# Kernel optimization log

Hardware: AMD Instinct MI355X
Metric: run time of the kernel (lower is better)

The kernel has to match this reference:

```python
import jax, jax.numpy as jnp
import numpy as np

N = 50000
E = 800000
IN_C = 256
HID = 256
OUT_C = 64
HEADS = 4
NEG_SLOPE = 0.2  # PyG GATConv default leaky_relu slope


def gat_conv(x, edge_index, W, a_src, a_dst, bias, heads, concat):
    """PyG-style GATConv (add_self_loops=True, eval mode so no dropout).
    x: [N, F_in]; W: [F_in, heads*C]; a_src/a_dst: [heads, C]; bias: [heads*C] or [C].
    """
    n = x.shape[0]
    # add self loops
    loops = jnp.arange(n, dtype=edge_index.dtype)
    src = jnp.concatenate([edge_index[0], loops])
    dst = jnp.concatenate([edge_index[1], loops])
    h = (x @ W).reshape(n, heads, -1)               # [N, H, C]
    alpha_src = jnp.einsum('nhc,hc->nh', h, a_src)  # [N, H]
    alpha_dst = jnp.einsum('nhc,hc->nh', h, a_dst)
    e = jax.nn.leaky_relu(alpha_src[src] + alpha_dst[dst], NEG_SLOPE)  # [E', H]
    # segment softmax over incoming edges of each dst node
    m = jax.ops.segment_max(e, dst, num_segments=n)        # [N, H]
    w = jnp.exp(e - m[dst])
    denom = jax.ops.segment_sum(w, dst, num_segments=n)    # [N, H]
    att = w / (denom[dst] + 1e-16)                          # [E', H]
    out = jax.ops.segment_sum(h[src] * att[:, :, None], dst, num_segments=n)  # [N, H, C]
    out = out.reshape(n, -1) if concat else out.mean(axis=1)
    return out + bias


def setup_inputs() -> dict:
    key = jax.random.key(0)
    ks = jax.random.split(key, 10)
    c1 = HID // HEADS  # per-head channels of layer 1
    s_in = 1.0 / np.sqrt(IN_C)
    s_hid = 1.0 / np.sqrt(HID)
    return {
        'x': jax.random.normal(ks[0], (N, IN_C), dtype=jnp.float32),
        'edge_index': jax.random.randint(ks[1], (2, E), 0, N, dtype=jnp.int64),
        'W1': jax.random.normal(ks[2], (IN_C, HEADS * c1), dtype=jnp.float32) * s_in,
        'a_src1': jax.random.normal(ks[3], (HEADS, c1), dtype=jnp.float32) * s_in,
        'a_dst1': jax.random.normal(ks[4], (HEADS, c1), dtype=jnp.float32) * s_in,
        'b1': jnp.zeros((HEADS * c1,), dtype=jnp.float32),
        'W2': jax.random.normal(ks[5], (HID, OUT_C), dtype=jnp.float32) * s_hid,
        'a_src2': jax.random.normal(ks[6], (1, OUT_C), dtype=jnp.float32) * s_hid,
        'a_dst2': jax.random.normal(ks[7], (1, OUT_C), dtype=jnp.float32) * s_hid,
        'b2': jnp.zeros((OUT_C,), dtype=jnp.float32),
    }


def reference(x, edge_index, W1, a_src1, a_dst1, b1, W2, a_src2, a_dst2, b2):
    h = gat_conv(x, edge_index, W1, a_src1, a_dst1, b1, heads=HEADS, concat=True)
    h = jax.nn.elu(h)
    # dropout: eval mode -> identity
    return gat_conv(h, edge_index, W2, a_src2, a_dst2, b2, heads=1, concat=False)
```

## Files before the change

kernel.cpp:

```cpp
#include <hip/hip_runtime.h>
#include <math.h>

#define NN 50000
#define NE 800000
#define ET (NE + NN)
#define FIN 256
#define HIDC 256
#define OC 64
#define NH 4
#define NEG 0.2f
#define CAP 64
#define NSTRIPES (NN / 16)
#define NGROUPS ((NSTRIPES + 1) / 2)

typedef __attribute__((ext_vector_type(8))) short bf16x8;
typedef __attribute__((ext_vector_type(4))) float f32x4;

__device__ __forceinline__ unsigned short f2bf(float f) {
    unsigned u = __float_as_uint(f);
    unsigned r = (u + 0x7FFFu + ((u >> 16) & 1u)) >> 16;
    return (unsigned short)r;
}
__device__ __forceinline__ float bflo(unsigned v) { return __uint_as_float(v << 16); }
__device__ __forceinline__ float bfhi(unsigned v) { return __uint_as_float(v & 0xffff0000u); }

__global__ void k_scatter(const int* __restrict__ ei, int* __restrict__ cnt,
                          unsigned short* __restrict__ esrc) {
    int e = blockIdx.x * blockDim.x + threadIdx.x;
    if (e >= ET) return;
    int s, d;
    if (e < NE) { s = ei[e]; d = ei[NE + e]; } else { s = d = e - NE; }
    int k = atomicAdd(&cnt[d], 1);
    if (k < CAP) esrc[(size_t)d * CAP + k] = (unsigned short)s;
}

__global__ void k_cvt(const float* __restrict__ x, unsigned short* __restrict__ xb,
                      int n) {
    int i = (blockIdx.x * 256 + threadIdx.x) * 8;
    if (i >= n) return;
    float4 f0 = *(const float4*)&x[i];
    float4 f1 = *(const float4*)&x[i + 4];
    uint4 o;
    o.x = (unsigned)f2bf(f0.x) | ((unsigned)f2bf(f0.y) << 16);
    o.y = (unsigned)f2bf(f0.z) | ((unsigned)f2bf(f0.w) << 16);
    o.z = (unsigned)f2bf(f1.x) | ((unsigned)f2bf(f1.y) << 16);
    o.w = (unsigned)f2bf(f1.z) | ((unsigned)f2bf(f1.w) << 16);
    *(uint4*)&xb[i] = o;
}

__global__ void k_pack(const float* __restrict__ W, unsigned short* __restrict__ Bp,
                       int N, int NTL, int total) {
    int t = blockIdx.x * 256 + threadIdx.x;
    if (t >= total) return;
    int lane = t & 63;
    int ntl = (t >> 6) % NTL;
    int ks = ((t >> 6) / NTL) & 7;
    int hy = t / (64 * NTL * 8);
    int col = hy * NTL * 16 + ntl * 16 + (lane & 15);
    int k0 = ks * 32 + (lane >> 4) * 8;
#pragma unroll
    for (int i = 0; i < 8; i++) Bp[(size_t)t * 8 + i] = f2bf(W[(k0 + i) * N + col]);
}

template <int NTL, int NHEADS>
__global__ void __launch_bounds__(256) k_gemm(const unsigned short* __restrict__ A,
                                              const unsigned short* __restrict__ Bp,
                                              unsigned short* __restrict__ D, int N,
                                              const float* __restrict__ aS,
                                              const float* __restrict__ aD,
                                              float* __restrict__ asOut,
                                              float* __restrict__ adOut) {
    constexpr int TOT = 8 * NTL * 64 * 8;
    constexpr int HPH = (NTL * 16) / 64;
    __shared__ unsigned short lds[TOT];
    const unsigned short* src = Bp + (size_t)blockIdx.y * TOT;
    for (int i = threadIdx.x * 8; i < TOT; i += 256 * 8)
        *(uint4*)&lds[i] = *(const uint4*)&src[i];
    __syncthreads();
    int wave = threadIdx.x >> 6, lane = threadIdx.x & 63;
    int l15 = lane & 15, lh = lane >> 4;
    int coloff = blockIdx.y * NTL * 16;
    float aSv[NTL], aDv[NTL];
#pragma unroll
    for (int nt = 0; nt < NTL; nt++) {
        aSv[nt] = aS[coloff + nt * 16 + l15];
        aDv[nt] = aD[coloff + nt * 16 + l15];
    }
    for (int g = blockIdx.x * 4 + wave; g < NGROUPS; g += gridDim.x * 4) {
        int st0 = g * 2;
        bool two = (st0 + 1 < NSTRIPES);
        const unsigned short* arow0 = A + (size_t)(st0 * 16 + l15) * 256 + lh * 8;
        const unsigned short* arow1 = two ? arow0 + 16 * 256 : arow0;
        bf16x8 a0[8], a1[8];
#pragma unroll
        for (int ks = 0; ks < 8; ks++) a0[ks] = *(const bf16x8*)(arow0 + ks * 32);
#pragma unroll
        for (int ks = 0; ks < 8; ks++) a1[ks] = *(const bf16x8*)(arow1 + ks * 32);
        f32x4 acc[2][NTL];
#pragma unroll
        for (int m = 0; m < 2; m++)
#pragma unroll
            for (int t = 0; t < NTL; t++) acc[m][t] = (f32x4){0.f, 0.f, 0.f, 0.f};
#pragma unroll
        for (int ks = 0; ks < 8; ks++) {
#pragma unroll
            for (int nt = 0; nt < NTL; nt++) {
                bf16x8 b = *(const bf16x8*)&lds[((size_t)(ks * NTL + nt) * 64 + lane) * 8];
                acc[0][nt] = __builtin_amdgcn_mfma_f32_16x16x32_bf16(a0[ks], b, acc[0][nt], 0, 0, 0);
                acc[1][nt] = __builtin_amdgcn_mfma_f32_16x16x32_bf16(a1[ks], b, acc[1][nt], 0, 0, 0);
            }
        }
        int nm = two ? 2 : 1;
        for (int m = 0; m < nm; m++) {
            int strow = (st0 + m) * 16;
            unsigned short* dbase = D + (size_t)strow * N + coloff;
#pragma unroll
            for (int nt = 0; nt < NTL; nt++)
#pragma unroll
                for (int r = 0; r < 4; r++)
                    dbase[(lh * 4 + r) * N + nt * 16 + l15] = f2bf(acc[m][nt][r]);
#pragma unroll
            for (int r = 0; r < 4; r++) {
#pragma unroll
                for (int gg = 0; gg < HPH; gg++) {
                    float ps = 0.f, pd = 0.f;
#pragma unroll
                    for (int q = 0; q < 4; q++) {
                        int nt = gg * 4 + q;
                        ps += acc[m][nt][r] * aSv[nt];
                        pd += acc[m][nt][r] * aDv[nt];
                    }
#pragma unroll
                    for (int off = 1; off < 16; off <<= 1) {
                        ps += __shfl_xor(ps, off);
                        pd += __shfl_xor(pd, off);
                    }
                    if (l15 == 0) {
                        int row = strow + lh * 4 + r;
                        int hidx = blockIdx.y * HPH + gg;
                        asOut[row * NHEADS + hidx] = ps;
                        adOut[row * NHEADS + hidx] = pd;
                    }
                }
            }
        }
    }
}


__global__ void k_agg1f(const int* __restrict__ cnt, const unsigned short* __restrict__ esrc,
                        const unsigned short* __restrict__ h, const float* __restrict__ as,
                        const float* __restrict__ ad, const float* __restrict__ bias,
                        unsigned short* __restrict__ out) {
    __shared__ float wlds[4][64][4];
    int wave = threadIdx.x >> 6;
    int n = blockIdx.x * 4 + wave;
    int lane = threadIdx.x & 63;
    if (n >= NN) return;
    int deg = cnt[n];
    deg = deg < CAP ? deg : CAP;
    const unsigned short* bucket = &esrc[(size_t)n * CAP];
    bool act = lane < deg;
    int myS = act ? (int)bucket[lane] : 0;
    float4 adv = *(const float4*)&ad[n * NH];
    float e0 = -INFINITY, e1 = -INFINITY, e2 = -INFINITY, e3 = -INFINITY;
    if (act) {
        float4 av = *(const float4*)&as[myS * NH];
        e0 = av.x + adv.x; e0 = e0 > 0.f ? e0 : NEG * e0;
        e1 = av.y + adv.y; e1 = e1 > 0.f ? e1 : NEG * e1;
        e2 = av.z + adv.z; e2 = e2 > 0.f ? e2 : NEG * e2;
        e3 = av.w + adv.w; e3 = e3 > 0.f ? e3 : NEG * e3;
    }
    float m0 = e0, m1 = e1, m2 = e2, m3 = e3;
    for (int off = 32; off; off >>= 1) {
        m0 = fmaxf(m0, __shfl_xor(m0, off));
        m1 = fmaxf(m1, __shfl_xor(m1, off));
        m2 = fmaxf(m2, __shfl_xor(m2, off));
        m3 = fmaxf(m3, __shfl_xor(m3, off));
    }
    float w0 = act ? expf(e0 - m0) : 0.f;
    float w1 = act ? expf(e1 - m1) : 0.f;
    float w2 = act ? expf(e2 - m2) : 0.f;
    float w3 = act ? expf(e3 - m3) : 0.f;
    *(float4*)&wlds[wave][lane][0] = (float4){w0, w1, w2, w3};
    float s0 = w0, s1 = w1, s2 = w2, s3 = w3;
    for (int off = 32; off; off >>= 1) {
        s0 += __shfl_xor(s0, off);
        s1 += __shfl_xor(s1, off);
        s2 += __shfl_xor(s2, off);
        s3 += __shfl_xor(s3, off);
    }
    int hh = lane >> 4;
    int cbase = hh * 64 + (lane & 15) * 4;
    float ssel = hh == 0 ? s0 : hh == 1 ? s1 : hh == 2 ? s2 : s3;
    float rsel = 1.f / (ssel + 1e-16f);
    const float* wcol = &wlds[wave][0][hh];
    const unsigned short* hb = h + cbase;
    float acc0 = 0.f, acc1 = 0.f, acc2 = 0.f, acc3 = 0.f;
    int degP = (deg + 7) & ~7;
    for (int j = 0; j < degP; j += 8) {
        uint2 pv[8];
        float wj[8];
#pragma unroll
        for (int u = 0; u < 8; u++) {
            int s = __shfl(myS, j + u);
            wj[u] = wcol[(j + u) * 4];
            pv[u] = *(const uint2*)&hb[(size_t)s * HIDC];
        }
#pragma unroll
        for (int u = 0; u < 8; u++) {
            acc0 += wj[u] * bflo(pv[u].x);
            acc1 += wj[u] * bfhi(pv[u].x);
            acc2 += wj[u] * bflo(pv[u].y);
            acc3 += wj[u] * bfhi(pv[u].y);
        }
    }
    float4 bv = *(const float4*)&bias[cbase];
    float v0 = acc0 * rsel + bv.x; v0 = v0 > 0.f ? v0 : expm1f(v0);
    float v1 = acc1 * rsel + bv.y; v1 = v1 > 0.f ? v1 : expm1f(v1);
    float v2 = acc2 * rsel + bv.z; v2 = v2 > 0.f ? v2 : expm1f(v2);
    float v3 = acc3 * rsel + bv.w; v3 = v3 > 0.f ? v3 : expm1f(v3);
    uint2 ov;
    ov.x = (unsigned)f2bf(v0) | ((unsigned)f2bf(v1) << 16);
    ov.y = (unsigned)f2bf(v2) | ((unsigned)f2bf(v3) << 16);
    *(uint2*)&out[(size_t)n * HIDC + cbase] = ov;
}

__global__ void k_agg2f(const int* __restrict__ cnt, const unsigned short* __restrict__ esrc,
                        const unsigned short* __restrict__ h, const float* __restrict__ as,
                        const float* __restrict__ ad, const float* __restrict__ bias,
                        float* __restrict__ out) {
    __shared__ float wlds[4][64];
    int wave = threadIdx.x >> 6;
    int n = blockIdx.x * 4 + wave;
    int lane = threadIdx.x & 63;
    if (n >= NN) return;
    int deg = cnt[n];
    deg = deg < CAP ? deg : CAP;
    const unsigned short* bucket = &esrc[(size_t)n * CAP];
    bool act = lane < deg;
    int myS = act ? (int)bucket[lane] : 0;
    float adv = ad[n];
    float e = -INFINITY;
    if (act) {
        e = as[myS] + adv;
        e = e > 0.f ? e : NEG * e;
    }
    float m = e;
    for (int off = 32; off; off >>= 1) m = fmaxf(m, __shfl_xor(m, off));
    float w = act ? expf(e - m) : 0.f;
    wlds[wave][lane] = w;
    float s = w;
    for (int off = 32; off; off >>= 1) s += __shfl_xor(s, off);
    float rd = 1.f / (s + 1e-16f);

    int sub = lane >> 4;
    int cw = (lane & 15) * 4;
    const unsigned short* hb = h + cw;
    float acc0 = 0.f, acc1 = 0.f, acc2 = 0.f, acc3 = 0.f;
    int degP = (deg + 7) & ~7;
    for (int j = 0; j < degP; j += 8) {
        uint2 pv[2];
        float wj[2];
#pragma unroll
        for (int u = 0; u < 2; u++) {
            int jj = j + u * 4 + sub;
            int sj = __shfl(myS, jj);
            wj[u] = wlds[wave][jj];
            pv[u] = *(const uint2*)&hb[(size_t)sj * OC];
        }
#pragma unroll
        for (int u = 0; u < 2; u++) {
            acc0 += wj[u] * bflo(pv[u].x);
            acc1 += wj[u] * bfhi(pv[u].x);
            acc2 += wj[u] * bflo(pv[u].y);
            acc3 += wj[u] * bfhi(pv[u].y);
        }
    }
#pragma unroll
    for (int off = 16; off < 64; off <<= 1) {
        acc0 += __shfl_xor(acc0, off);
        acc1 += __shfl_xor(acc1, off);
        acc2 += __shfl_xor(acc2, off);
        acc3 += __shfl_xor(acc3, off);
    }
    if (lane < 16) {
        float4 bv = *(const float4*)&bias[cw];
        float4 o;
        o.x = acc0 * rd + bv.x;
        o.y = acc1 * rd + bv.y;
        o.z = acc2 * rd + bv.z;
        o.w = acc3 * rd + bv.w;
        *(float4*)&out[(size_t)n * OC + cw] = o;
    }
}

extern "C" void kernel_launch(void* const* d_in, const int* in_sizes, int n_in,
                              void* d_out, int out_size, void* d_ws, size_t ws_size,
                              hipStream_t stream) {
    const float* x   = (const float*)d_in[0];
    const int*   ei  = (const int*)d_in[1];
    const float* W1  = (const float*)d_in[2];
    const float* aS1 = (const float*)d_in[3];
    const float* aD1 = (const float*)d_in[4];
    const float* b1  = (const float*)d_in[5];
    const float* W2  = (const float*)d_in[6];
    const float* aS2 = (const float*)d_in[7];
    const float* aD2 = (const float*)d_in[8];
    const float* b2  = (const float*)d_in[9];
    float* out = (float*)d_out;

    char* p = (char*)d_ws;
    auto alloc = [&](size_t nbytes) {
        char* r = p;
        p += (nbytes + 255) & ~(size_t)255;
        return r;
    };
    unsigned short* xb    = (unsigned short*)alloc((size_t)NN * FIN * 2);
    unsigned short* h1b   = (unsigned short*)alloc((size_t)NN * HIDC * 2);
    unsigned short* act1b = (unsigned short*)alloc((size_t)NN * HIDC * 2);
    unsigned short* h2b   = (unsigned short*)alloc((size_t)NN * OC * 2);
    unsigned short* Bp1   = (unsigned short*)alloc((size_t)2 * 8 * 8 * 64 * 8 * 2);
    unsigned short* Bp2   = (unsigned short*)alloc((size_t)1 * 8 * 4 * 64 * 8 * 2);
    float* as1  = (float*)alloc((size_t)NN * NH * 4);
    float* ad1  = (float*)alloc((size_t)NN * NH * 4);
    float* as2  = (float*)alloc((size_t)NN * 4);
    float* ad2  = (float*)alloc((size_t)NN * 4);
    int*   cnt  = (int*)alloc((size_t)NN * 4);
    unsigned short* esrc = (unsigned short*)alloc((size_t)NN * CAP * 2);

    hipMemsetAsync(cnt, 0, (size_t)NN * 4, stream);

    k_scatter<<<(ET + 255) / 256, 256, 0, stream>>>(ei, cnt, esrc);
    k_cvt<<<(NN * FIN / 8 + 255) / 256, 256, 0, stream>>>(x, xb, NN * FIN);
    k_pack<<<(2 * 8 * 8 * 64 + 255) / 256, 256, 0, stream>>>(W1, Bp1, HIDC, 8, 2 * 8 * 8 * 64);
    k_pack<<<(1 * 8 * 4 * 64 + 255) / 256, 256, 0, stream>>>(W2, Bp2, OC, 4, 1 * 8 * 4 * 64);

    k_gemm<8, NH><<<dim3(196, 2), 256, 0, stream>>>(xb, Bp1, h1b, HIDC, aS1, aD1, as1, ad1);
    k_agg1f<<<(NN + 3) / 4, 256, 0, stream>>>(cnt, esrc, h1b, as1, ad1, b1, act1b);

    k_gemm<4, 1><<<dim3(196, 1), 256, 0, stream>>>(act1b, Bp2, h2b, OC, aS2, aD2, as2, ad2);
    k_agg2f<<<(NN + 3) / 4, 256, 0, stream>>>(cnt, esrc, h2b, as2, ad2, b2, out);
}
```

Baseline: 226.8 us.

## Split layer-1 aggregation into attention-weight kernel and channel-sliced gather kernel

The fused layer-1 aggregation kernel is split in two. The first kernel computes the softmax attention weights and reciprocal denominators per node and writes them to a new global buffer laid out per head. The second kernel gathers neighbor features with each block covering a 32-channel slice of 8 nodes. This raises parallelism and shrinks the per-thread gather width, which may improve locality of the source-row gathers across slices. The cost is an extra launch, a roughly 51 MB weight buffer written and read back, and narrower 4-byte loads per lane.

```diff
diff --git a/kernel.cpp b/kernel.cpp
--- a/kernel.cpp
+++ b/kernel.cpp
@@ -147,25 +147,21 @@
     }
 }
 
-
-__global__ void k_agg1f(const int* __restrict__ cnt, const unsigned short* __restrict__ esrc,
-                        const unsigned short* __restrict__ h, const float* __restrict__ as,
-                        const float* __restrict__ ad, const float* __restrict__ bias,
-                        unsigned short* __restrict__ out) {
-    __shared__ float wlds[4][64][4];
+__global__ void k_attn1(const int* __restrict__ cnt, const unsigned short* __restrict__ esrc,
+                        const float* __restrict__ as, const float* __restrict__ ad,
+                        float* __restrict__ watt, float* __restrict__ rden) {
     int wave = threadIdx.x >> 6;
     int n = blockIdx.x * 4 + wave;
-    int lane = threadIdx.x & 63;
+    int j = threadIdx.x & 63;
     if (n >= NN) return;
     int deg = cnt[n];
     deg = deg < CAP ? deg : CAP;
-    const unsigned short* bucket = &esrc[(size_t)n * CAP];
-    bool act = lane < deg;
-    int myS = act ? (int)bucket[lane] : 0;
+    bool act = j < deg;
+    int s = act ? (int)esrc[(size_t)n * CAP + j] : 0;
     float4 adv = *(const float4*)&ad[n * NH];
     float e0 = -INFINITY, e1 = -INFINITY, e2 = -INFINITY, e3 = -INFINITY;
     if (act) {
-        float4 av = *(const float4*)&as[myS * NH];
+        float4 av = *(const float4*)&as[s * NH];
         e0 = av.x + adv.x; e0 = e0 > 0.f ? e0 : NEG * e0;
         e1 = av.y + adv.y; e1 = e1 > 0.f ? e1 : NEG * e1;
         e2 = av.z + adv.z; e2 = e2 > 0.f ? e2 : NEG * e2;
@@ -182,7 +178,11 @@
     float w1 = act ? expf(e1 - m1) : 0.f;
     float w2 = act ? expf(e2 - m2) : 0.f;
     float w3 = act ? expf(e3 - m3) : 0.f;
-    *(float4*)&wlds[wave][lane][0] = (float4){w0, w1, w2, w3};
+    size_t base = (size_t)n * CAP + j;
+    watt[base] = w0;
+    watt[(size_t)NN * CAP + base] = w1;
+    watt[(size_t)2 * NN * CAP + base] = w2;
+    watt[(size_t)3 * NN * CAP + base] = w3;
     float s0 = w0, s1 = w1, s2 = w2, s3 = w3;
     for (int off = 32; off; off >>= 1) {
         s0 += __shfl_xor(s0, off);
@@ -190,40 +190,56 @@
         s2 += __shfl_xor(s2, off);
         s3 += __shfl_xor(s3, off);
     }
-    int hh = lane >> 4;
-    int cbase = hh * 64 + (lane & 15) * 4;
-    float ssel = hh == 0 ? s0 : hh == 1 ? s1 : hh == 2 ? s2 : s3;
-    float rsel = 1.f / (ssel + 1e-16f);
-    const float* wcol = &wlds[wave][0][hh];
+    if (j == 0)
+        *(float4*)&rden[n * NH] = (float4){1.f / (s0 + 1e-16f), 1.f / (s1 + 1e-16f),
+                                           1.f / (s2 + 1e-16f), 1.f / (s3 + 1e-16f)};
+}
+
+__global__ void k_agg1s(const int* __restrict__ cnt, const unsigned short* __restrict__ esrc,
+                        const unsigned short* __restrict__ h, const float* __restrict__ watt,
+                        const float* __restrict__ rden, const float* __restrict__ bias,
+                        unsigned short* __restrict__ out) {
+    int slice = blockIdx.x & 7;
+    int g = blockIdx.x >> 3;
+    int wave = threadIdx.x >> 6, lane = threadIdx.x & 63;
+    int half = lane >> 5, l31 = lane & 31;
+    int n = g * 8 + wave * 2 + half;
+    if (n >= NN) return;
+    int hh = slice >> 1;
+    int deg = cnt[n];
+    deg = deg < CAP ? deg : CAP;
+    const unsigned short* bucket = &esrc[(size_t)n * CAP];
+    int myS0 = (l31 < deg) ? (int)bucket[l31] : 0;
+    int myS1 = (32 + l31 < deg) ? (int)bucket[32 + l31] : 0;
+    const float* wrow = watt + ((size_t)hh * NN + n) * CAP;
+    float rsel = rden[n * NH + hh];
+    int sub = l31 >> 4;
+    int cbase = slice * 32 + (l31 & 15) * 2;
     const unsigned short* hb = h + cbase;
-    float acc0 = 0.f, acc1 = 0.f, acc2 = 0.f, acc3 = 0.f;
-    int degP = (deg + 7) & ~7;
-    for (int j = 0; j < degP; j += 8) {
-        uint2 pv[8];
-        float wj[8];
-#pragma unroll
-        for (int u = 0; u < 8; u++) {
-            int s = __shfl(myS, j + u);
-            wj[u] = wcol[(j + u) * 4];
-            pv[u] = *(const uint2*)&hb[(size_t)s * HIDC];
-        }
-#pragma unroll
-        for (int u = 0; u < 8; u++) {
-            acc0 += wj[u] * bflo(pv[u].x);
-            acc1 += wj[u] * bfhi(pv[u].x);
-            acc2 += wj[u] * bflo(pv[u].y);
-            acc3 += wj[u] * bfhi(pv[u].y);
-        }
-    }
-    float4 bv = *(const float4*)&bias[cbase];
-    float v0 = acc0 * rsel + bv.x; v0 = v0 > 0.f ? v0 : expm1f(v0);
-    float v1 = acc1 * rsel + bv.y; v1 = v1 > 0.f ? v1 : expm1f(v1);
-    float v2 = acc2 * rsel + bv.z; v2 = v2 > 0.f ? v2 : expm1f(v2);
-    float v3 = acc3 * rsel + bv.w; v3 = v3 > 0.f ? v3 : expm1f(v3);
-    uint2 ov;
-    ov.x = (unsigned)f2bf(v0) | ((unsigned)f2bf(v1) << 16);
-    ov.y = (unsigned)f2bf(v2) | ((unsigned)f2bf(v3) << 16);
-    *(uint2*)&out[(size_t)n * HIDC + cbase] = ov;
+    float acc0 = 0.f, acc1 = 0.f;
+    int degP = (deg + 3) & ~3;
+    for (int j = 0; j < degP; j += 4) {
+#pragma unroll
+        for (int u = 0; u < 2; u++) {
+            int jj = j + u * 2 + sub;
+            int sel = jj & 31;
+            int sA = __shfl(myS0, sel, 32);
+            int sB = __shfl(myS1, sel, 32);
+            int s = (jj < 32) ? sA : sB;
+            float wj = wrow[jj];
+            unsigned pv = *(const unsigned*)&hb[(size_t)s * HIDC];
+            acc0 += wj * bflo(pv);
+            acc1 += wj * bfhi(pv);
+        }
+    }
+    acc0 += __shfl_xor(acc0, 16);
+    acc1 += __shfl_xor(acc1, 16);
+    if (sub == 0) {
+        float v0 = acc0 * rsel + bias[cbase];     v0 = v0 > 0.f ? v0 : expm1f(v0);
+        float v1 = acc1 * rsel + bias[cbase + 1]; v1 = v1 > 0.f ? v1 : expm1f(v1);
+        *(unsigned*)&out[(size_t)n * HIDC + cbase] =
+            (unsigned)f2bf(v0) | ((unsigned)f2bf(v1) << 16);
+    }
 }
 
 __global__ void k_agg2f(const int* __restrict__ cnt, const unsigned short* __restrict__ esrc,
@@ -322,8 +338,10 @@
     unsigned short* h2b   = (unsigned short*)alloc((size_t)NN * OC * 2);
     unsigned short* Bp1   = (unsigned short*)alloc((size_t)2 * 8 * 8 * 64 * 8 * 2);
     unsigned short* Bp2   = (unsigned short*)alloc((size_t)1 * 8 * 4 * 64 * 8 * 2);
+    float* watt = (float*)alloc((size_t)NH * NN * CAP * 4);
     float* as1  = (float*)alloc((size_t)NN * NH * 4);
     float* ad1  = (float*)alloc((size_t)NN * NH * 4);
+    float* rd1  = (float*)alloc((size_t)NN * NH * 4);
     float* as2  = (float*)alloc((size_t)NN * 4);
     float* ad2  = (float*)alloc((size_t)NN * 4);
     int*   cnt  = (int*)alloc((size_t)NN * 4);
@@ -337,7 +355,8 @@
     k_pack<<<(1 * 8 * 4 * 64 + 255) / 256, 256, 0, stream>>>(W2, Bp2, OC, 4, 1 * 8 * 4 * 64);
 
     k_gemm<8, NH><<<dim3(196, 2), 256, 0, stream>>>(xb, Bp1, h1b, HIDC, aS1, aD1, as1, ad1);
-    k_agg1f<<<(NN + 3) / 4, 256, 0, stream>>>(cnt, esrc, h1b, as1, ad1, b1, act1b);
+    k_attn1<<<(NN + 3) / 4, 256, 0, stream>>>(cnt, esrc, as1, ad1, watt, rd1);
+    k_agg1s<<<((NN + 7) / 8) * 8, 256, 0, stream>>>(cnt, esrc, h1b, watt, rd1, b1, act1b);
 
     k_gemm<4, 1><<<dim3(196, 1), 256, 0, stream>>>(act1b, Bp2, h2b, OC, aS2, aD2, as2, ad2);
     k_agg2f<<<(NN + 3) / 4, 256, 0, stream>>>(cnt, esrc, h2b, as2, ad2, b2, out);
```

Result: slower. 303.4 us (+33.8%).
